# Performance work log

Measured on AMD Instinct MI355X. Metric: run time of the kernel, lower is better.

## Reference

```python
import jax, jax.numpy as jnp
import numpy as np

D = 2048          # input_dim == dec_hidden_size
S = 16384         # src_time_steps
H = 250           # projection hidden (hard-coded in module)


def setup_inputs() -> dict:
    key = jax.random.key(0)
    ks = jax.random.split(key, 12)
    sc_d = 1.0 / np.sqrt(D)
    sc_3d = 1.0 / np.sqrt(3 * D)
    sc_h = 1.0 / np.sqrt(H)
    return {
        "s_prev": jax.random.normal(ks[0], (1, 1, D), jnp.float32),
        "enc_hs": jax.random.normal(ks[1], (1, S, D), jnp.float32),
        "cur_men_rep": jax.random.normal(ks[2], (1, 1, D), jnp.float32),
        "src_mask": jax.random.randint(ks[3], (1, S), 0, 2, jnp.int32),
        "W_info": jax.random.normal(ks[4], (D, D), jnp.float32) * sc_d,
        "W_ctx": jax.random.normal(ks[5], (D, D), jnp.float32) * sc_d,
        "W_q": jax.random.normal(ks[6], (D, D), jnp.float32) * sc_d,
        "b_q": jnp.zeros((D,), jnp.float32),
        "W_p1": jax.random.normal(ks[7], (H, 3 * D), jnp.float32) * sc_3d,
        "b_p1": jnp.zeros((H,), jnp.float32),
        "W_p2": jax.random.normal(ks[8], (1, H), jnp.float32) * sc_h,
        "b_p2": jnp.zeros((1,), jnp.float32),
    }


def reference(s_prev, enc_hs, cur_men_rep, src_mask,
              W_info, W_ctx, W_q, b_q, W_p1, b_p1, W_p2, b_p2):
    # dh = linear_info(cur_men_rep): [1,1,D]; uh = linear_ctx(enc_hs): [1,S,D]
    dh = jnp.einsum('bqe,de->bqd', cur_men_rep, W_info)
    uh = jnp.einsum('bse,de->bsd', enc_hs, W_ctx)
    wq = jnp.einsum('bqe,de->bqd', s_prev, W_q) + b_q
    # cat(uh, wq.repeat, dh.repeat) -> tanh : [1,S,3D]
    wquh = jnp.tanh(jnp.concatenate(
        [uh, jnp.broadcast_to(wq, uh.shape), jnp.broadcast_to(dh, uh.shape)],
        axis=2))
    # projection: Linear(3D,250) -> Dropout(eval: identity) -> ReLU -> Linear(250,1)
    h = jax.nn.relu(jnp.einsum('bsk,hk->bsh', wquh, W_p1) + b_p1)
    scores = (jnp.einsum('bsh,oh->bso', h, W_p2) + b_p2).squeeze()   # [S] (B=1)
    scores = jnp.where(src_mask.squeeze().astype(bool), -jnp.inf, scores)
    attn = jax.nn.softmax(scores, axis=-1)                            # [S]
    ctx = jnp.sum(enc_hs * attn[None, :, None], axis=1)               # [1,D]
    return attn, ctx
```

## Files before the change

kernel.cpp:

```cpp
#include <hip/hip_runtime.h>
#include <hip/hip_bf16.h>
#include <stdint.h>

#define DD 2048
#define SS 16384
#define HH 250
#define GEMMB_GRID 264

typedef __attribute__((ext_vector_type(8))) short bf16x8;
typedef __attribute__((ext_vector_type(4))) float f32x4;

__device__ __forceinline__ unsigned short f2bf(float f){
  union { float f; uint32_t u; } v; v.f = f;
  uint32_t u = v.u;
  return (unsigned short)((u + 0x7fffu + ((u >> 16) & 1u)) >> 16);
}
__device__ __forceinline__ float fast_tanh(float x){
  return 1.0f - 2.0f / (1.0f + __expf(2.0f * x));
}
__device__ __forceinline__ void gl_lds16(const void* g, void* l){
  __builtin_amdgcn_global_load_lds((const __attribute__((address_space(1))) void*)g,
                                   (__attribute__((address_space(3))) void*)l, 16, 0, 0);
}

__global__ __launch_bounds__(256) void mega_kernel(
    const float* __restrict__ W_ctx, unsigned short* __restrict__ wctxb,
    const float* __restrict__ W_p1, unsigned short* __restrict__ wp1ab,
    const float* __restrict__ s_prev, const float* __restrict__ cmr,
    const float* __restrict__ Wq, const float* __restrict__ bq,
    const float* __restrict__ Winfo,
    float* __restrict__ twq, float* __restrict__ tdh,
    const int* __restrict__ mask, int* __restrict__ idx, int* __restrict__ cpos,
    int* __restrict__ mcount)
{
  const int b = blockIdx.x, t = threadIdx.x;
  if(b < 512){
    for(int i = b * 256 + t; i < (DD * DD) / 8; i += 512 * 256){
      const float4* p = (const float4*)(W_ctx + (size_t)i * 8);
      float4 a = p[0], c = p[1];
      bf16x8 v;
      v[0]=(short)f2bf(a.x); v[1]=(short)f2bf(a.y); v[2]=(short)f2bf(a.z); v[3]=(short)f2bf(a.w);
      v[4]=(short)f2bf(c.x); v[5]=(short)f2bf(c.y); v[6]=(short)f2bf(c.z); v[7]=(short)f2bf(c.w);
      *(bf16x8*)(wctxb + (size_t)i * 8) = v;
    }
  } else if(b < 768){
    int g = (b - 512) * 256 + t;
    int row = g >> 8, col = (g & 255) * 8;
    int rc = row < HH ? row : HH - 1;
    const float* s = W_p1 + (size_t)rc * (3 * DD) + col;
    bf16x8 v;
    #pragma unroll
    for(int j = 0; j < 8; j++) v[j] = (row < HH) ? (short)f2bf(s[j]) : (short)0;
    *(bf16x8*)(wp1ab + (size_t)g * 8) = v;
  } else if(b < 1792){
    int vb = b - 768;
    int wid = t >> 6, lane = t & 63;
    bool isq = vb < 512;
    int r = (isq ? vb : vb - 512) * 4 + wid;
    const float* M = (isq ? Wq : Winfo) + (size_t)r * DD;
    const float* x = isq ? s_prev : cmr;
    float s = 0.f;
    for(int i = lane; i < DD; i += 64) s += M[i] * x[i];
    #pragma unroll
    for(int o = 32; o; o >>= 1) s += __shfl_xor(s, o);
    if(lane == 0){
      if(isq) twq[r] = fast_tanh(s + bq[r]);
      else    tdh[r] = fast_tanh(s);
    }
  } else {
    __shared__ int cnt[256];
    const int base = t * 64;
    int c = 0;
    for(int i = 0; i < 64; i++) c += (mask[base + i] == 0);
    cnt[t] = c;
    __syncthreads();
    for(int off = 1; off < 256; off <<= 1){
      int v = (t >= off) ? cnt[t - off] : 0;
      __syncthreads();
      cnt[t] += v;
      __syncthreads();
    }
    int p = cnt[t] - c;
    for(int i = 0; i < 64; i++){
      int fi = base + i;
      if(mask[fi] == 0){ idx[p] = fi; cpos[fi] = p; p++; }
      else cpos[fi] = -1;
    }
    if(t == 255){
      int tot = cnt[255];
      mcount[0] = tot;
      mcount[1] = (tot + 255) & ~255;
      mcount[2] = (tot + 63) & ~63;
    }
  }
}

__global__ __launch_bounds__(256) void conv_enc_kernel(
    const float* __restrict__ enc, const int* __restrict__ idx,
    const int* __restrict__ mcount, unsigned short* __restrict__ out,
    const float* __restrict__ wp1, const float* __restrict__ bp1,
    const float* __restrict__ twq, const float* __restrict__ tdh,
    float* __restrict__ bias2)
{
  const int b = blockIdx.x, t = threadIdx.x;
  if(b < 2048){
    const int mc0 = mcount[0], mc1 = mcount[1];
    #pragma unroll
    for(int r = 0; r < 8; r++){
      int j = b * 8 + r;
      if(j >= mc1) return;
      unsigned short* o = out + (size_t)j * DD + t * 8;
      if(j >= mc0){
        bf16x8 z;
        #pragma unroll
        for(int i = 0; i < 8; i++) z[i] = 0;
        *(bf16x8*)o = z;
      } else {
        const float4* p = (const float4*)(enc + (size_t)idx[j] * DD + t * 8);
        float4 a = p[0], c = p[1];
        bf16x8 v;
        v[0]=(short)f2bf(a.x); v[1]=(short)f2bf(a.y); v[2]=(short)f2bf(a.z); v[3]=(short)f2bf(a.w);
        v[4]=(short)f2bf(c.x); v[5]=(short)f2bf(c.y); v[6]=(short)f2bf(c.z); v[7]=(short)f2bf(c.w);
        *(bf16x8*)o = v;
      }
    }
  } else {
    int h = (b - 2048) * 4 + (t >> 6);
    int lane = t & 63;
    if(h >= HH){ if(lane == 0 && h < 256) bias2[h] = 0.f; return; }
    const float* r1 = wp1 + (size_t)h * (3 * DD) + DD;
    const float* r2 = wp1 + (size_t)h * (3 * DD) + 2 * DD;
    float s = 0.f;
    for(int i = lane; i < DD; i += 64) s += r1[i] * twq[i] + r2[i] * tdh[i];
    #pragma unroll
    for(int o = 32; o; o >>= 1) s += __shfl_xor(s, o);
    if(lane == 0) bias2[h] = s + bp1[h];
  }
}

__device__ __forceinline__ void stage_half(const unsigned short* __restrict__ g,
                                           int grow0, int kt, char* ldsbase,
                                           int wid, int lane)
{
  const int srow = lane >> 3;
  const int c = (lane & 7) ^ srow;
  #pragma unroll
  for(int i = 0; i < 2; i++){
    int r8 = (wid * 2 + i) * 8;
    gl_lds16(g + (size_t)(grow0 + r8 + srow) * DD + kt + c * 8,
             ldsbase + r8 * 128);
  }
}
#define RDF(base, lr, kc) (*(const bf16x8*)((base) + (lr) * 128 + (((kc) * 16) ^ (((lr) & 7) << 4))))

__global__ __launch_bounds__(512, 2) void gemmA_kernel(
    const unsigned short* __restrict__ A, const unsigned short* __restrict__ B,
    const int* __restrict__ mcount, unsigned short* __restrict__ Ct)
{
  __shared__ alignas(128) char lds[131072];
  const int tid = threadIdx.x, lane = tid & 63, wid = tid >> 6;
  const int wm = wid >> 2, wn = wid & 3;
  const int slot = blockIdx.x >> 3;
  const int mt = (blockIdx.x & 7) + ((slot >> 3) << 3);
  const int n0 = (slot & 7) * 256;
  const int MT = mcount[1] >> 8;
  if(mt >= MT) return;
  const int m0 = mt * 256;
  const int frow = lane & 15, kch = lane >> 4;

  f32x4 acc[8][4] = {};

  stage_half(A, m0,        0, lds,                 wid, lane);
  stage_half(A, m0 + 128,  0, lds + 16384,         wid, lane);
  stage_half(B, n0,        0, lds + 32768,         wid, lane);
  stage_half(B, n0 + 128,  0, lds + 49152,         wid, lane);
  stage_half(B, n0,       64, lds + 65536 + 32768, wid, lane);
  stage_half(B, n0 + 128, 64, lds + 65536 + 49152, wid, lane);
  asm volatile("s_waitcnt vmcnt(4)" ::: "memory");
  __builtin_amdgcn_s_barrier();

  #pragma unroll 2
  for(int t = 0; t < 32; t++){
    const int d = t & 1;
    char* Ab = lds + d * 65536;
    char* Bb = Ab + 32768;
    char* An = lds + (d ^ 1) * 65536;
    bf16x8 bfr[4][2];
    #pragma unroll
    for(int q = 0; q < 4; q++){
      if(q == 0){
        #pragma unroll
        for(int nr = 0; nr < 4; nr++){
          int row = wn * 64 + nr * 16 + frow;
          #pragma unroll
          for(int ks = 0; ks < 2; ks++) bfr[nr][ks] = RDF(Bb, row, ks * 4 + kch);
        }
      }
      bf16x8 afr[2][2];
      #pragma unroll
      for(int mi = 0; mi < 2; mi++){
        int row = wm * 128 + (q * 2 + mi) * 16 + frow;
        #pragma unroll
        for(int ks = 0; ks < 2; ks++) afr[mi][ks] = RDF(Ab, row, ks * 4 + kch);
      }
      if(q == 0){
        if(t + 1 < 32){
          stage_half(A, m0,       (t + 1) * 64, An,         wid, lane);
          stage_half(A, m0 + 128, (t + 1) * 64, An + 16384, wid, lane);
        }
      } else if(q == 1){
        if(t + 2 < 32) stage_half(B, n0,       (t + 2) * 64, Bb,         wid, lane);
      } else if(q == 2){
        if(t + 2 < 32) stage_half(B, n0 + 128, (t + 2) * 64, Bb + 16384, wid, lane);
      }
      __builtin_amdgcn_s_barrier();
      __builtin_amdgcn_sched_barrier(0);
      __builtin_amdgcn_s_setprio(1);
      #pragma unroll
      for(int mi = 0; mi < 2; mi++)
        #pragma unroll
        for(int nr = 0; nr < 4; nr++)
          #pragma unroll
          for(int ks = 0; ks < 2; ks++)
            acc[q * 2 + mi][nr] = __builtin_amdgcn_mfma_f32_16x16x32_bf16(
                afr[mi][ks], bfr[nr][ks], acc[q * 2 + mi][nr], 0, 0, 0);
      __builtin_amdgcn_s_setprio(0);
      __builtin_amdgcn_sched_barrier(0);
      if(q == 3){
        if(t < 30)       asm volatile("s_waitcnt vmcnt(4)" ::: "memory");
        else if(t == 30) asm volatile("s_waitcnt vmcnt(0)" ::: "memory");
      }
      __builtin_amdgcn_s_barrier();
    }
  }

  const int r0 = m0 + wm * 128 + (lane >> 4) * 4;
  const int c0 = n0 + wn * 64 + frow;
  #pragma unroll
  for(int mr = 0; mr < 8; mr++)
    #pragma unroll
    for(int nr = 0; nr < 4; nr++)
      #pragma unroll
      for(int r = 0; r < 4; r++)
        Ct[(size_t)(r0 + mr * 16 + r) * DD + c0 + nr * 16] = f2bf(fast_tanh(acc[mr][nr][r]));
}

__global__ __launch_bounds__(512, 4) void gemmB_kernel(
    const unsigned short* __restrict__ A, const unsigned short* __restrict__ B,
    const int* __restrict__ mcount, const float* __restrict__ bias2,
    const float* __restrict__ w2, const float* __restrict__ bp2,
    float* __restrict__ attnc, float* __restrict__ Tpart)
{
  __shared__ alignas(128) char lds[81920];
  __shared__ float sred[8][32];
  const int tid = threadIdx.x, lane = tid & 63, wid = tid >> 6;
  const int wm = wid >> 2, wn = wid & 3;
  const int m0 = blockIdx.x * 64;
  const int mc0 = mcount[0], mc2 = mcount[2];
  if(m0 >= mc2){ if(tid == 0) Tpart[blockIdx.x] = 0.f; return; }
  const int frow = lane & 15, kch = lane >> 4;
  const int srow = lane >> 3, sc = ((lane & 7) ^ srow) * 8;

  f32x4 acc[2][4] = {};

  gl_lds16(A + (size_t)(m0 + wid * 8 + srow) * DD + sc, lds + wid * 1024);
  #pragma unroll
  for(int i = 0; i < 4; i++){
    int l = wid + 8 * i;
    gl_lds16(B + (size_t)(l * 8 + srow) * DD + sc,      lds + 16384 + l * 1024);
    gl_lds16(B + (size_t)(l * 8 + srow) * DD + 64 + sc, lds + 49152 + l * 1024);
  }
  asm volatile("s_waitcnt vmcnt(4)" ::: "memory");
  __builtin_amdgcn_s_barrier();

  #pragma unroll 2
  for(int t = 0; t < 32; t++){
    const int d = t & 1;
    char* Ab = lds + d * 8192;
    char* An = lds + (d ^ 1) * 8192;
    char* Bb = lds + 16384 + d * 32768;
    bf16x8 bfr[4][2], afr[2];
    #pragma unroll
    for(int q = 0; q < 2; q++){
      if(q == 0){
        #pragma unroll
        for(int nr = 0; nr < 4; nr++){
          int row = wn * 64 + nr * 16 + frow;
          #pragma unroll
          for(int ks = 0; ks < 2; ks++) bfr[nr][ks] = RDF(Bb, row, ks * 4 + kch);
        }
      }
      {
        int row = wm * 32 + q * 16 + frow;
        #pragma unroll
        for(int ks = 0; ks < 2; ks++) afr[ks] = RDF(Ab, row, ks * 4 + kch);
      }
      if(q == 0){
        if(t + 1 < 32)
          gl_lds16(A + (size_t)(m0 + wid * 8 + srow) * DD + (t + 1) * 64 + sc, An + wid * 1024);
      } else {
        if(t + 2 < 32){
          #pragma unroll
          for(int i = 0; i < 4; i++){
            int l = wid + 8 * i;
            gl_lds16(B + (size_t)(l * 8 + srow) * DD + (t + 2) * 64 + sc, Bb + l * 1024);
          }
        }
      }
      __builtin_amdgcn_s_barrier();
      __builtin_amdgcn_sched_barrier(0);
      __builtin_amdgcn_s_setprio(1);
      #pragma unroll
      for(int nr = 0; nr < 4; nr++)
        #pragma unroll
        for(int ks = 0; ks < 2; ks++)
          acc[q][nr] = __builtin_amdgcn_mfma_f32_16x16x32_bf16(afr[ks], bfr[nr][ks], acc[q][nr], 0, 0, 0);
      __builtin_amdgcn_s_setprio(0);
      __builtin_amdgcn_sched_barrier(0);
      if(q == 1){
        if(t < 30)       asm volatile("s_waitcnt vmcnt(4)" ::: "memory");
        else if(t == 30) asm volatile("s_waitcnt vmcnt(0)" ::: "memory");
      }
      __builtin_amdgcn_s_barrier();
    }
  }

  float w2v[4], b2v[4];
  #pragma unroll
  for(int in = 0; in < 4; in++){
    int n = wn * 64 + in * 16 + frow;
    w2v[in] = (n < HH) ? w2[n] : 0.f;
    b2v[in] = bias2[n];
  }
  #pragma unroll
  for(int mi = 0; mi < 2; mi++){
    #pragma unroll
    for(int r = 0; r < 4; r++){
      float s = 0.f;
      #pragma unroll
      for(int in = 0; in < 4; in++){
        float h = acc[mi][in][r] + b2v[in];
        s += (h > 0.f ? h : 0.f) * w2v[in];
      }
      s += __shfl_xor(s, 1); s += __shfl_xor(s, 2);
      s += __shfl_xor(s, 4); s += __shfl_xor(s, 8);
      if(frow == 0) sred[wid][mi * 16 + (lane >> 4) * 4 + r] = s;
    }
  }
  __syncthreads();
  if(tid < 64){
    int wmr = tid >> 5, rr = tid & 31;
    float s = sred[wmr * 4][rr] + sred[wmr * 4 + 1][rr] + sred[wmr * 4 + 2][rr]
            + sred[wmr * 4 + 3][rr] + bp2[0];
    int j = m0 + tid;
    float e = (j < mc0) ? __expf(s) : 0.f;
    if(j < mc0) attnc[j] = e;
    #pragma unroll
    for(int o = 32; o; o >>= 1) e += __shfl_xor(e, o);
    if(tid == 0) Tpart[blockIdx.x] = e;
  }
}

__global__ __launch_bounds__(256) void norm_kernel(
    const float* __restrict__ attnc, const int* __restrict__ cpos,
    const float* __restrict__ Tpart, float* __restrict__ out)
{
  __shared__ float sT;
  if(threadIdx.x == 0){
    float s = 0.f;
    for(int i = 0; i < GEMMB_GRID; i++) s += Tpart[i];
    sT = 1.0f / s;
  }
  __syncthreads();
  int i = blockIdx.x * 256 + threadIdx.x;
  int cp = cpos[i];
  out[i] = (cp >= 0) ? attnc[cp] * sT : 0.f;
}

__device__ __forceinline__ float bf2f(unsigned short h){
  union { uint32_t u; float f; } v; v.u = ((uint32_t)h) << 16; return v.f;
}
__global__ __launch_bounds__(256) void ctxp_kernel(
    const float* __restrict__ attnc, const unsigned short* __restrict__ encb,
    const int* __restrict__ mcount, float* __restrict__ part)
{
  const int b = blockIdx.x, t = threadIdx.x;
  const int mc0 = mcount[0];
  const int chunk = (mc0 + 255) >> 8;
  const int j0 = b * chunk;
  const int j1 = min(j0 + chunk, mc0);
  float a[8] = {};
  for(int j = j0; j < j1; j++){
    float e = attnc[j];
    bf16x8 v = *(const bf16x8*)(encb + (size_t)j * DD + t * 8);
    #pragma unroll
    for(int k = 0; k < 8; k++) a[k] += e * bf2f((unsigned short)v[k]);
  }
  float* o = part + (size_t)b * DD + t * 8;
  #pragma unroll
  for(int k = 0; k < 8; k++) o[k] = a[k];
}

__global__ __launch_bounds__(256) void ctxr_kernel(
    const float* __restrict__ part, const float* __restrict__ Tpart,
    float* __restrict__ out)
{
  __shared__ float sT;
  if(threadIdx.x == 0){
    float s = 0.f;
    for(int i = 0; i < GEMMB_GRID; i++) s += Tpart[i];
    sT = 1.0f / s;
  }
  __syncthreads();
  const int dcol = blockIdx.x * 256 + threadIdx.x;
  float s = 0.f;
  for(int b = 0; b < 256; b++) s += part[(size_t)b * DD + dcol];
  out[dcol] = s * sT;
}

extern "C" void kernel_launch(void* const* d_in, const int* in_sizes, int n_in,
                              void* d_out, int out_size, void* d_ws, size_t ws_size,
                              hipStream_t stream)
{
  const float* s_prev = (const float*)d_in[0];
  const float* enc    = (const float*)d_in[1];
  const float* cmr    = (const float*)d_in[2];
  const int*   mask   = (const int*)d_in[3];
  const float* W_info = (const float*)d_in[4];
  const float* W_ctx  = (const float*)d_in[5];
  const float* W_q    = (const float*)d_in[6];
  const float* b_q    = (const float*)d_in[7];
  const float* W_p1   = (const float*)d_in[8];
  const float* b_p1   = (const float*)d_in[9];
  const float* W_p2   = (const float*)d_in[10];
  const float* b_p2   = (const float*)d_in[11];
  float* out = (float*)d_out;

  char* ws = (char*)d_ws;
  unsigned short* encb    = (unsigned short*)(ws);
  unsigned short* tanhbuf = (unsigned short*)(ws + 67108864);
  unsigned short* wctxb   = (unsigned short*)(ws + 134217728);
  unsigned short* wp1ab   = (unsigned short*)(ws + 142606336);
  int*   idx    = (int*)(ws + 143654912);
  int*   cpos   = (int*)(ws + 143720448);
  float* attnc  = (float*)(ws + 143785984);
  float* part   = (float*)(ws + 143851520);
  float* twq    = (float*)(ws + 145948672);
  float* tdh    = (float*)(ws + 145956864);
  float* bias2  = (float*)(ws + 145965056);
  int*   mcount = (int*)(ws + 145966080);
  float* Tpart  = (float*)(ws + 145966208);

  mega_kernel<<<1793, 256, 0, stream>>>(W_ctx, wctxb, W_p1, wp1ab,
                                        s_prev, cmr, W_q, b_q, W_info,
                                        twq, tdh, mask, idx, cpos, mcount);
  conv_enc_kernel<<<2112, 256, 0, stream>>>(enc, idx, mcount, encb,
                                            W_p1, b_p1, twq, tdh, bias2);
  gemmA_kernel<<<512, 512, 0, stream>>>(encb, wctxb, mcount, tanhbuf);
  gemmB_kernel<<<GEMMB_GRID, 512, 0, stream>>>(tanhbuf, wp1ab, mcount, bias2,
                                               W_p2, b_p2, attnc, Tpart);
  norm_kernel<<<64, 256, 0, stream>>>(attnc, cpos, Tpart, out);
  ctxp_kernel<<<256, 256, 0, stream>>>(attnc, encb, mcount, part);
  ctxr_kernel<<<8, 256, 0, stream>>>(part, Tpart, out + SS);
}
```

Measured before the change: 194.3 us.

## Convert all encoder rows densely and gather unmasked rows inside GEMM loads

The encoder fp32→bf16 conversion moves into the first kernel and now covers every row, so it no longer has to wait for the mask compaction. gemmA instead looks up each tile row through the idx array and loads it directly into LDS. The bias2 projection is folded into extra gemmA blocks, and the normalisation and context-partial kernels are merged into one launch. Together these remove two kernel launches and one serial dependency. The cost is converting and writing roughly twice as many encoder rows, since masked rows are now converted too, and using indirect, less regular row addresses in the GEMM staging and context pass.

Result: slower. 222.3 us (+14.5%).

```diff
diff --git a/kernel.cpp b/kernel.cpp
--- a/kernel.cpp
+++ b/kernel.cpp
@@ -14,6 +14,9 @@
   union { float f; uint32_t u; } v; v.f = f;
   uint32_t u = v.u;
   return (unsigned short)((u + 0x7fffu + ((u >> 16) & 1u)) >> 16);
+}
+__device__ __forceinline__ float bf2f(unsigned short h){
+  union { uint32_t u; float f; } v; v.u = ((uint32_t)h) << 16; return v.f;
 }
 __device__ __forceinline__ float fast_tanh(float x){
   return 1.0f - 2.0f / (1.0f + __expf(2.0f * x));
@@ -31,43 +34,11 @@
     const float* __restrict__ Winfo,
     float* __restrict__ twq, float* __restrict__ tdh,
     const int* __restrict__ mask, int* __restrict__ idx, int* __restrict__ cpos,
-    int* __restrict__ mcount)
+    int* __restrict__ mcount,
+    const float* __restrict__ enc, unsigned short* __restrict__ encb)
 {
   const int b = blockIdx.x, t = threadIdx.x;
-  if(b < 512){
-    for(int i = b * 256 + t; i < (DD * DD) / 8; i += 512 * 256){
-      const float4* p = (const float4*)(W_ctx + (size_t)i * 8);
-      float4 a = p[0], c = p[1];
-      bf16x8 v;
-      v[0]=(short)f2bf(a.x); v[1]=(short)f2bf(a.y); v[2]=(short)f2bf(a.z); v[3]=(short)f2bf(a.w);
-      v[4]=(short)f2bf(c.x); v[5]=(short)f2bf(c.y); v[6]=(short)f2bf(c.z); v[7]=(short)f2bf(c.w);
-      *(bf16x8*)(wctxb + (size_t)i * 8) = v;
-    }
-  } else if(b < 768){
-    int g = (b - 512) * 256 + t;
-    int row = g >> 8, col = (g & 255) * 8;
-    int rc = row < HH ? row : HH - 1;
-    const float* s = W_p1 + (size_t)rc * (3 * DD) + col;
-    bf16x8 v;
-    #pragma unroll
-    for(int j = 0; j < 8; j++) v[j] = (row < HH) ? (short)f2bf(s[j]) : (short)0;
-    *(bf16x8*)(wp1ab + (size_t)g * 8) = v;
-  } else if(b < 1792){
-    int vb = b - 768;
-    int wid = t >> 6, lane = t & 63;
-    bool isq = vb < 512;
-    int r = (isq ? vb : vb - 512) * 4 + wid;
-    const float* M = (isq ? Wq : Winfo) + (size_t)r * DD;
-    const float* x = isq ? s_prev : cmr;
-    float s = 0.f;
-    for(int i = lane; i < DD; i += 64) s += M[i] * x[i];
-    #pragma unroll
-    for(int o = 32; o; o >>= 1) s += __shfl_xor(s, o);
-    if(lane == 0){
-      if(isq) twq[r] = fast_tanh(s + bq[r]);
-      else    tdh[r] = fast_tanh(s);
-    }
-  } else {
+  if(b == 0){
     __shared__ int cnt[256];
     const int base = t * 64;
     int c = 0;
@@ -92,41 +63,91 @@
       mcount[1] = (tot + 255) & ~255;
       mcount[2] = (tot + 63) & ~63;
     }
-  }
-}
-
-__global__ __launch_bounds__(256) void conv_enc_kernel(
-    const float* __restrict__ enc, const int* __restrict__ idx,
-    const int* __restrict__ mcount, unsigned short* __restrict__ out,
+  } else if(b < 2049){
+    #pragma unroll
+    for(int r = 0; r < 8; r++){
+      int j = (b - 1) * 8 + r;
+      const float4* p = (const float4*)(enc + (size_t)j * DD + t * 8);
+      float4 a = p[0], c = p[1];
+      bf16x8 v;
+      v[0]=(short)f2bf(a.x); v[1]=(short)f2bf(a.y); v[2]=(short)f2bf(a.z); v[3]=(short)f2bf(a.w);
+      v[4]=(short)f2bf(c.x); v[5]=(short)f2bf(c.y); v[6]=(short)f2bf(c.z); v[7]=(short)f2bf(c.w);
+      *(bf16x8*)(encb + (size_t)j * DD + t * 8) = v;
+    }
+  } else if(b < 2561){
+    for(int i = (b - 2049) * 256 + t; i < (DD * DD) / 8; i += 512 * 256){
+      const float4* p = (const float4*)(W_ctx + (size_t)i * 8);
+      float4 a = p[0], c = p[1];
+      bf16x8 v;
+      v[0]=(short)f2bf(a.x); v[1]=(short)f2bf(a.y); v[2]=(short)f2bf(a.z); v[3]=(short)f2bf(a.w);
+      v[4]=(short)f2bf(c.x); v[5]=(short)f2bf(c.y); v[6]=(short)f2bf(c.z); v[7]=(short)f2bf(c.w);
+      *(bf16x8*)(wctxb + (size_t)i * 8) = v;
+    }
+  } else if(b < 2817){
+    int g = (b - 2561) * 256 + t;
+    int row = g >> 8, col = (g & 255) * 8;
+    int rc = row < HH ? row : HH - 1;
+    const float* s = W_p1 + (size_t)rc * (3 * DD) + col;
+    bf16x8 v;
+    #pragma unroll
+    for(int j = 0; j < 8; j++) v[j] = (row < HH) ? (short)f2bf(s[j]) : (short)0;
+    *(bf16x8*)(wp1ab + (size_t)g * 8) = v;
+  } else {
+    int vb = b - 2817;
+    int wid = t >> 6, lane = t & 63;
+    bool isq = vb < 512;
+    int r = (isq ? vb : vb - 512) * 4 + wid;
+    const float* M = (isq ? Wq : Winfo) + (size_t)r * DD;
+    const float* x = isq ? s_prev : cmr;
+    float s = 0.f;
+    for(int i = lane; i < DD; i += 64) s += M[i] * x[i];
+    #pragma unroll
+    for(int o = 32; o; o >>= 1) s += __shfl_xor(s, o);
+    if(lane == 0){
+      if(isq) twq[r] = fast_tanh(s + bq[r]);
+      else    tdh[r] = fast_tanh(s);
+    }
+  }
+}
+
+__device__ __forceinline__ void stageA_idx(const unsigned short* __restrict__ g,
+                                           const int* r2, int kt, char* ldsbase,
+                                           int wid, int lane)
+{
+  const int srow = lane >> 3;
+  const int c = (lane & 7) ^ srow;
+  #pragma unroll
+  for(int i = 0; i < 2; i++){
+    int r8 = (wid * 2 + i) * 8;
+    gl_lds16(g + (size_t)r2[i] * DD + kt + c * 8, ldsbase + r8 * 128);
+  }
+}
+__device__ __forceinline__ void stage_half(const unsigned short* __restrict__ g,
+                                           int grow0, int kt, char* ldsbase,
+                                           int wid, int lane)
+{
+  const int srow = lane >> 3;
+  const int c = (lane & 7) ^ srow;
+  #pragma unroll
+  for(int i = 0; i < 2; i++){
+    int r8 = (wid * 2 + i) * 8;
+    gl_lds16(g + (size_t)(grow0 + r8 + srow) * DD + kt + c * 8,
+             ldsbase + r8 * 128);
+  }
+}
+#define RDF(base, lr, kc) (*(const bf16x8*)((base) + (lr) * 128 + (((kc) * 16) ^ (((lr) & 7) << 4))))
+
+__global__ __launch_bounds__(512, 2) void gemmA_kernel(
+    const unsigned short* __restrict__ A, const int* __restrict__ idx,
+    const unsigned short* __restrict__ B, const int* __restrict__ mcount,
+    unsigned short* __restrict__ Ct,
     const float* __restrict__ wp1, const float* __restrict__ bp1,
     const float* __restrict__ twq, const float* __restrict__ tdh,
     float* __restrict__ bias2)
 {
-  const int b = blockIdx.x, t = threadIdx.x;
-  if(b < 2048){
-    const int mc0 = mcount[0], mc1 = mcount[1];
-    #pragma unroll
-    for(int r = 0; r < 8; r++){
-      int j = b * 8 + r;
-      if(j >= mc1) return;
-      unsigned short* o = out + (size_t)j * DD + t * 8;
-      if(j >= mc0){
-        bf16x8 z;
-        #pragma unroll
-        for(int i = 0; i < 8; i++) z[i] = 0;
-        *(bf16x8*)o = z;
-      } else {
-        const float4* p = (const float4*)(enc + (size_t)idx[j] * DD + t * 8);
-        float4 a = p[0], c = p[1];
-        bf16x8 v;
-        v[0]=(short)f2bf(a.x); v[1]=(short)f2bf(a.y); v[2]=(short)f2bf(a.z); v[3]=(short)f2bf(a.w);
-        v[4]=(short)f2bf(c.x); v[5]=(short)f2bf(c.y); v[6]=(short)f2bf(c.z); v[7]=(short)f2bf(c.w);
-        *(bf16x8*)o = v;
-      }
-    }
-  } else {
-    int h = (b - 2048) * 4 + (t >> 6);
-    int lane = t & 63;
+  const int tid = threadIdx.x, lane = tid & 63, wid = tid >> 6;
+  if(blockIdx.x >= 512){
+    int h = (blockIdx.x - 512) * 8 + wid;
     if(h >= HH){ if(lane == 0 && h < 256) bias2[h] = 0.f; return; }
     const float* r1 = wp1 + (size_t)h * (3 * DD) + DD;
     const float* r2 = wp1 + (size_t)h * (3 * DD) + 2 * DD;
@@ -135,30 +156,9 @@
     #pragma unroll
     for(int o = 32; o; o >>= 1) s += __shfl_xor(s, o);
     if(lane == 0) bias2[h] = s + bp1[h];
-  }
-}
-
-__device__ __forceinline__ void stage_half(const unsigned short* __restrict__ g,
-                                           int grow0, int kt, char* ldsbase,
-                                           int wid, int lane)
-{
-  const int srow = lane >> 3;
-  const int c = (lane & 7) ^ srow;
-  #pragma unroll
-  for(int i = 0; i < 2; i++){
-    int r8 = (wid * 2 + i) * 8;
-    gl_lds16(g + (size_t)(grow0 + r8 + srow) * DD + kt + c * 8,
-             ldsbase + r8 * 128);
-  }
-}
-#define RDF(base, lr, kc) (*(const bf16x8*)((base) + (lr) * 128 + (((kc) * 16) ^ (((lr) & 7) << 4))))
-
-__global__ __launch_bounds__(512, 2) void gemmA_kernel(
-    const unsigned short* __restrict__ A, const unsigned short* __restrict__ B,
-    const int* __restrict__ mcount, unsigned short* __restrict__ Ct)
-{
+    return;
+  }
   __shared__ alignas(128) char lds[131072];
-  const int tid = threadIdx.x, lane = tid & 63, wid = tid >> 6;
   const int wm = wid >> 2, wn = wid & 3;
   const int slot = blockIdx.x >> 3;
   const int mt = (blockIdx.x & 7) + ((slot >> 3) << 3);
@@ -168,10 +168,23 @@
   const int m0 = mt * 256;
   const int frow = lane & 15, kch = lane >> 4;
 
+  int ra0[2], ra1[2];
+  {
+    const int tot = mcount[0];
+    const int srow = lane >> 3;
+    #pragma unroll
+    for(int i = 0; i < 2; i++){
+      int r0 = m0 + (wid * 2 + i) * 8 + srow;
+      int r1 = r0 + 128;
+      ra0[i] = idx[r0 < tot ? r0 : tot - 1];
+      ra1[i] = idx[r1 < tot ? r1 : tot - 1];
+    }
+  }
+
   f32x4 acc[8][4] = {};
 
-  stage_half(A, m0,        0, lds,                 wid, lane);
-  stage_half(A, m0 + 128,  0, lds + 16384,         wid, lane);
+  stageA_idx(A, ra0, 0, lds,         wid, lane);
+  stageA_idx(A, ra1, 0, lds + 16384, wid, lane);
   stage_half(B, n0,        0, lds + 32768,         wid, lane);
   stage_half(B, n0 + 128,  0, lds + 49152,         wid, lane);
   stage_half(B, n0,       64, lds + 65536 + 32768, wid, lane);
@@ -205,8 +218,8 @@
       }
       if(q == 0){
         if(t + 1 < 32){
-          stage_half(A, m0,       (t + 1) * 64, An,         wid, lane);
-          stage_half(A, m0 + 128, (t + 1) * 64, An + 16384, wid, lane);
+          stageA_idx(A, ra0, (t + 1) * 64, An,         wid, lane);
+          stageA_idx(A, ra1, (t + 1) * 64, An + 16384, wid, lane);
         }
       } else if(q == 1){
         if(t + 2 < 32) stage_half(B, n0,       (t + 2) * 64, Bb,         wid, lane);
@@ -361,44 +374,41 @@
   }
 }
 
-__global__ __launch_bounds__(256) void norm_kernel(
+__global__ __launch_bounds__(256) void normctx_kernel(
     const float* __restrict__ attnc, const int* __restrict__ cpos,
-    const float* __restrict__ Tpart, float* __restrict__ out)
-{
-  __shared__ float sT;
-  if(threadIdx.x == 0){
-    float s = 0.f;
-    for(int i = 0; i < GEMMB_GRID; i++) s += Tpart[i];
-    sT = 1.0f / s;
-  }
-  __syncthreads();
-  int i = blockIdx.x * 256 + threadIdx.x;
-  int cp = cpos[i];
-  out[i] = (cp >= 0) ? attnc[cp] * sT : 0.f;
-}
-
-__device__ __forceinline__ float bf2f(unsigned short h){
-  union { uint32_t u; float f; } v; v.u = ((uint32_t)h) << 16; return v.f;
-}
-__global__ __launch_bounds__(256) void ctxp_kernel(
-    const float* __restrict__ attnc, const unsigned short* __restrict__ encb,
-    const int* __restrict__ mcount, float* __restrict__ part)
+    const int* __restrict__ idx, const int* __restrict__ mcount,
+    const float* __restrict__ Tpart, const unsigned short* __restrict__ encb,
+    float* __restrict__ out, float* __restrict__ part)
 {
   const int b = blockIdx.x, t = threadIdx.x;
-  const int mc0 = mcount[0];
-  const int chunk = (mc0 + 255) >> 8;
-  const int j0 = b * chunk;
-  const int j1 = min(j0 + chunk, mc0);
-  float a[8] = {};
-  for(int j = j0; j < j1; j++){
-    float e = attnc[j];
-    bf16x8 v = *(const bf16x8*)(encb + (size_t)j * DD + t * 8);
-    #pragma unroll
-    for(int k = 0; k < 8; k++) a[k] += e * bf2f((unsigned short)v[k]);
-  }
-  float* o = part + (size_t)b * DD + t * 8;
-  #pragma unroll
-  for(int k = 0; k < 8; k++) o[k] = a[k];
+  if(b < 64){
+    __shared__ float sT;
+    if(t == 0){
+      float s = 0.f;
+      for(int i = 0; i < GEMMB_GRID; i++) s += Tpart[i];
+      sT = 1.0f / s;
+    }
+    __syncthreads();
+    int i = b * 256 + t;
+    int cp = cpos[i];
+    out[i] = (cp >= 0) ? attnc[cp] * sT : 0.f;
+  } else {
+    const int bb = b - 64;
+    const int mc0 = mcount[0];
+    const int chunk = (mc0 + 255) >> 8;
+    const int j0 = bb * chunk;
+    const int j1 = min(j0 + chunk, mc0);
+    float a[8] = {};
+    for(int j = j0; j < j1; j++){
+      float e = attnc[j];
+      bf16x8 v = *(const bf16x8*)(encb + (size_t)idx[j] * DD + t * 8);
+      #pragma unroll
+      for(int k = 0; k < 8; k++) a[k] += e * bf2f((unsigned short)v[k]);
+    }
+    float* o = part + (size_t)bb * DD + t * 8;
+    #pragma unroll
+    for(int k = 0; k < 8; k++) o[k] = a[k];
+  }
 }
 
 __global__ __launch_bounds__(256) void ctxr_kernel(
@@ -451,15 +461,15 @@
   int*   mcount = (int*)(ws + 145966080);
   float* Tpart  = (float*)(ws + 145966208);
 
-  mega_kernel<<<1793, 256, 0, stream>>>(W_ctx, wctxb, W_p1, wp1ab,
+  mega_kernel<<<3841, 256, 0, stream>>>(W_ctx, wctxb, W_p1, wp1ab,
                                         s_prev, cmr, W_q, b_q, W_info,
-                                        twq, tdh, mask, idx, cpos, mcount);
-  conv_enc_kernel<<<2112, 256, 0, stream>>>(enc, idx, mcount, encb,
-                                            W_p1, b_p1, twq, tdh, bias2);
-  gemmA_kernel<<<512, 512, 0, stream>>>(encb, wctxb, mcount, tanhbuf);
+                                        twq, tdh, mask, idx, cpos, mcount,
+                                        enc, encb);
+  gemmA_kernel<<<544, 512, 0, stream>>>(encb, idx, wctxb, mcount, tanhbuf,
+                                        W_p1, b_p1, twq, tdh, bias2);
   gemmB_kernel<<<GEMMB_GRID, 512, 0, stream>>>(tanhbuf, wp1ab, mcount, bias2,
                                                W_p2, b_p2, attnc, Tpart);
-  norm_kernel<<<64, 256, 0, stream>>>(attnc, cpos, Tpart, out);
-  ctxp_kernel<<<256, 256, 0, stream>>>(attnc, encb, mcount, part);
+  normctx_kernel<<<320, 256, 0, stream>>>(attnc, cpos, idx, mcount, Tpart,
+                                          encb, out, part);
   ctxr_kernel<<<8, 256, 0, stream>>>(part, Tpart, out + SS);
 }
```
